# Kernel tuning notes

Measured on AMD Instinct MI355X. Metric: run time of the kernel, lower is better.

Reference implementation:

```python
import jax, jax.numpy as jnp
import numpy as np

VOCAB = 25
HIDDEN = 512
B, S = 64, 2048


def setup_inputs() -> dict:
    key = jax.random.key(0)
    ks = jax.random.split(key, 8)
    tokens = jax.random.randint(ks[0], (B, S), 0, VOCAB)
    lengths = jax.random.randint(ks[1], (B,), 1, S + 1)  # pack_padded requires length >= 1
    k = 1.0 / np.sqrt(HIDDEN)
    u = lambda kk, shp: jax.random.uniform(kk, shp, jnp.float32, -k, k)
    return {
        "tokens": tokens,
        "lengths": lengths,
        "W_ih": u(ks[2], (4 * HIDDEN, VOCAB)),   # gate order i,f,g,o (PyTorch)
        "W_hh": u(ks[3], (4 * HIDDEN, HIDDEN)),
        "b_ih": u(ks[4], (4 * HIDDEN,)),
        "b_hh": u(ks[5], (4 * HIDDEN,)),
        "fc_w": u(ks[6], (1, HIDDEN)),
        "fc_b": u(ks[7], (1,)),
    }


def _lstm_last_hidden(x, lengths, W_ih, W_hh, b_ih, b_hh):
    # x: [B,S,V] one-hot; returns h at each sequence's last valid step (packed-LSTM semantics)
    b, s, _ = x.shape
    h0 = jnp.zeros((b, HIDDEN), x.dtype)
    c0 = jnp.zeros((b, HIDDEN), x.dtype)
    # precompute input projections for all steps: [S,B,4H]
    xg = jnp.einsum('bsv,gv->sbg', x, W_ih) + b_ih + b_hh

    def step(carry, inp):
        h, c = carry
        xt, t = inp
        gates = xt + h @ W_hh.T
        i, f, g, o = jnp.split(gates, 4, axis=-1)
        i = jax.nn.sigmoid(i); f = jax.nn.sigmoid(f)
        g = jnp.tanh(g); o = jax.nn.sigmoid(o)
        c_new = f * c + i * g
        h_new = o * jnp.tanh(c_new)
        m = (t < lengths)[:, None]  # freeze state past sequence end
        return (jnp.where(m, h_new, h), jnp.where(m, c_new, c)), None

    (h, _), _ = jax.lax.scan(step, (h0, c0), (xg, jnp.arange(s)))
    return h


def reference(tokens, lengths, W_ih, W_hh, b_ih, b_hh, fc_w, fc_b):
    # sort by length descending, like the torch forward (output stays in sorted order)
    order = jnp.argsort(-lengths)
    toks = tokens[order]
    lens = lengths[order]
    x = jax.nn.one_hot(toks, VOCAB, dtype=jnp.float32)  # fused one-hot (replaces python loop)
    h = _lstm_last_hidden(x, lens, W_ih, W_hh, b_ih, b_hh)
    return h @ fc_w.T + fc_b  # [B,1]
```

## Files before the change

kernel.cpp:

```cpp
#include <hip/hip_runtime.h>


#define VOCAB 25
#define HIDDEN 512
#define BATCH 64
#define SEQ 2048
#define GB 16
#define NG 4
#define WPG 16
#define HSL 32
#define RWG 128
#define NTHREADS 256
#define HGQ (GB * HIDDEN / 2)

typedef short s16x8 __attribute__((ext_vector_type(8)));
typedef float f32x4 __attribute__((ext_vector_type(4)));

__device__ inline unsigned short f2bf(float x) {
  unsigned u = __float_as_uint(x);
  u += 0x7fffu + ((u >> 16) & 1u);
  return (unsigned short)(u >> 16);
}
__device__ inline float sigf(float x) { return 1.0f / (1.0f + __expf(-x)); }
__device__ inline float tanh_fast(float x) { return 2.0f / (1.0f + __expf(-2.0f * x)) - 1.0f; }

__global__ void prep_kernel(unsigned long long* hg, float* out) {
  const int i = blockIdx.x * blockDim.x + threadIdx.x;
  const int n = blockDim.x * gridDim.x;
  for (int k = i; k < 2 * NG * HGQ; k += n) hg[k] = 0ull;
  if (i < BATCH) out[i] = 0.f;
}

__global__ __launch_bounds__(NTHREADS, 1) void lstm_persistent(
    const int* __restrict__ tokens, const int* __restrict__ lengths,
    const float* __restrict__ W_ih, const float* __restrict__ W_hh,
    const float* __restrict__ b_ih, const float* __restrict__ b_hh,
    const float* __restrict__ fc_w, const float* __restrict__ fc_b,
    float* __restrict__ out, unsigned long long* hg) {
  const int tid = threadIdx.x;
  const int bid = blockIdx.x;
  const int x = bid & 7;
  const int g = x >> 1;
  const int w = ((bid >> 3) << 1) | (x & 1);

  __shared__ __align__(16) unsigned short hbuf[GB][HIDDEN + 8];
  __shared__ float gatesb[GB][RWG + 4];
  __shared__ float xgt[VOCAB][RWG + 4];
  __shared__ int lenAll[BATCH];
  __shared__ int order_[BATCH];
  __shared__ int gIdx[GB];
  __shared__ int gLen[GB];

  if (tid < BATCH) lenAll[tid] = lengths[tid];
  __syncthreads();
  if (tid < BATCH) {
    const int L = lenAll[tid];
    int r = 0;
    for (int j = 0; j < BATCH; ++j) {
      const int lj = lenAll[j];
      r += ((lj > L) || (lj == L && j < tid)) ? 1 : 0;
    }
    order_[r] = tid;
  }
  __syncthreads();
  if (tid < GB) {
    const int oi = order_[g * GB + tid];
    gIdx[tid] = oi;
    gLen[tid] = lenAll[oi];
  }
  for (int i = tid; i < GB * (HIDDEN + 8); i += NTHREADS)
    ((unsigned short*)hbuf)[i] = 0;
  for (int i = tid; i < VOCAB * RWG; i += NTHREADS) {
    const int v = i / RWG, rl = i % RWG;
    const int rg = (rl >> 5) * HIDDEN + w * HSL + (rl & 31);
    xgt[v][rl] = W_ih[rg * VOCAB + v] + b_ih[rg] + b_hh[rg];
  }
  __syncthreads();

  const int T = gLen[0];
  const int lane = tid & 63;
  const int wv = tid >> 6;
  const int m16 = lane & 15;
  const int quad = lane >> 4;

  s16x8 Bf[2][16];
#pragma unroll
  for (int nti = 0; nti < 2; ++nti) {
    const int nt = wv + 4 * nti;
    const int rl = nt * 16 + m16;
    const int rg = (rl >> 5) * HIDDEN + w * HSL + (rl & 31);
    const float* wr = W_hh + (size_t)rg * HIDDEN;
#pragma unroll
    for (int kt = 0; kt < 16; ++kt) {
      const float* p = wr + kt * 32 + quad * 8;
#pragma unroll
      for (int e = 0; e < 8; ++e) Bf[nti][kt][e] = (short)f2bf(p[e]);
    }
  }

  const int cb = tid >> 4;
  const int cs = tid & 15;
  const int jj0 = 2 * cs, jj1 = 2 * cs + 1;
  const int myLen = gLen[cb];
  const int* tokRow = tokens + (size_t)gIdx[cb] * SEQ;
  unsigned long long* const base0 = hg + (size_t)g * HGQ;
  unsigned long long* const base1 = hg + (size_t)(NG + g) * HGQ;

  float c0 = 0.f, c1 = 0.f, h0 = 0.f, h1 = 0.f;

  for (int t = 0; t < T; ++t) {
    const int tok = tokRow[t];

    if (t > 0) {
      const unsigned long long* src = ((t & 1) ? base1 : base0) + tid;
      unsigned long long q[16];
      for (;;) {
        bool ok = true;
#pragma unroll
        for (int r = 0; r < 16; ++r)
          q[r] = __hip_atomic_load(src + r * 256, __ATOMIC_RELAXED,
                                   __HIP_MEMORY_SCOPE_AGENT);
#pragma unroll
        for (int r = 0; r < 16; ++r) ok &= ((unsigned)(q[r] >> 32) == (unsigned)t);
        if (ok) break;
        __builtin_amdgcn_s_sleep(1);
      }
#pragma unroll
      for (int r = 0; r < 16; ++r)
        *(unsigned*)&hbuf[cb][r * 32 + jj0] = (unsigned)q[r];
    }
    __syncthreads();

    f32x4 acc0a = {0.f, 0.f, 0.f, 0.f}, acc0b = {0.f, 0.f, 0.f, 0.f};
    f32x4 acc1a = {0.f, 0.f, 0.f, 0.f}, acc1b = {0.f, 0.f, 0.f, 0.f};
#pragma unroll
    for (int kt = 0; kt < 16; kt += 2) {
      const s16x8 A0 = *(const s16x8*)&hbuf[m16][kt * 32 + quad * 8];
      const s16x8 A1 = *(const s16x8*)&hbuf[m16][(kt + 1) * 32 + quad * 8];
      acc0a = __builtin_amdgcn_mfma_f32_16x16x32_bf16(A0, Bf[0][kt], acc0a, 0, 0, 0);
      acc1a = __builtin_amdgcn_mfma_f32_16x16x32_bf16(A0, Bf[1][kt], acc1a, 0, 0, 0);
      acc0b = __builtin_amdgcn_mfma_f32_16x16x32_bf16(A1, Bf[0][kt + 1], acc0b, 0, 0, 0);
      acc1b = __builtin_amdgcn_mfma_f32_16x16x32_bf16(A1, Bf[1][kt + 1], acc1b, 0, 0, 0);
    }
    const f32x4 acc0 = acc0a + acc0b;
    const f32x4 acc1 = acc1a + acc1b;
#pragma unroll
    for (int v = 0; v < 4; ++v) {
      gatesb[quad * 4 + v][wv * 16 + m16] = acc0[v];
      gatesb[quad * 4 + v][(wv + 4) * 16 + m16] = acc1[v];
    }
    __syncthreads();

    const float pi0 = gatesb[cb][jj0] + xgt[tok][jj0];
    const float pf0 = gatesb[cb][32 + jj0] + xgt[tok][32 + jj0];
    const float pg0 = gatesb[cb][64 + jj0] + xgt[tok][64 + jj0];
    const float po0 = gatesb[cb][96 + jj0] + xgt[tok][96 + jj0];
    const float pi1 = gatesb[cb][jj1] + xgt[tok][jj1];
    const float pf1 = gatesb[cb][32 + jj1] + xgt[tok][32 + jj1];
    const float pg1 = gatesb[cb][64 + jj1] + xgt[tok][64 + jj1];
    const float po1 = gatesb[cb][96 + jj1] + xgt[tok][96 + jj1];
    if (t < myLen) {
      const float i0 = sigf(pi0), f0 = sigf(pf0), g0 = tanh_fast(pg0), o0 = sigf(po0);
      c0 = f0 * c0 + i0 * g0;
      h0 = o0 * tanh_fast(c0);
      const float i1 = sigf(pi1), f1 = sigf(pf1), g1 = tanh_fast(pg1), o1 = sigf(po1);
      c1 = f1 * c1 + i1 * g1;
      h1 = o1 * tanh_fast(c1);
    }
    if (t + 1 < T) {
      const unsigned payload = (unsigned)f2bf(h0) | ((unsigned)f2bf(h1) << 16);
      const unsigned long long qv = ((unsigned long long)(unsigned)(t + 1) << 32) | payload;
      unsigned long long* hp = (((t + 1) & 1) ? base1 : base0) + w * 256 + tid;
      __hip_atomic_store(hp, qv, __ATOMIC_RELAXED, __HIP_MEMORY_SCOPE_AGENT);
    }
  }

  float part = h0 * fc_w[w * HSL + jj0] + h1 * fc_w[w * HSL + jj1];
  part += __shfl_down(part, 8, 16);
  part += __shfl_down(part, 4, 16);
  part += __shfl_down(part, 2, 16);
  part += __shfl_down(part, 1, 16);
  if (cs == 0) {
    if (w == 0) part += fc_b[0];
    atomicAdd(&out[g * GB + cb], part);
  }
}

extern "C" void kernel_launch(void* const* d_in, const int* in_sizes, int n_in,
                              void* d_out, int out_size, void* d_ws, size_t ws_size,
                              hipStream_t stream) {
  (void)in_sizes; (void)n_in; (void)out_size; (void)ws_size;
  const int* tokens = (const int*)d_in[0];
  const int* lengths = (const int*)d_in[1];
  const float* W_ih = (const float*)d_in[2];
  const float* W_hh = (const float*)d_in[3];
  const float* b_ih = (const float*)d_in[4];
  const float* b_hh = (const float*)d_in[5];
  const float* fc_w = (const float*)d_in[6];
  const float* fc_b = (const float*)d_in[7];
  float* out = (float*)d_out;
  unsigned long long* hglob = (unsigned long long*)d_ws;

  prep_kernel<<<32, 256, 0, stream>>>(hglob, out);
  lstm_persistent<<<64, NTHREADS, 0, stream>>>(tokens, lengths, W_ih, W_hh, b_ih, b_hh,
                                               fc_w, fc_b, out, hglob);
}
```

Baseline: 5.588 ms.

## Exchange hidden state through XCD-local L2 when a group's blocks share an XCD

The launch doubles to 128 blocks and odd-indexed ones exit at once, so the 64 working blocks land on a different spread of XCDs. Each block reads its XCC id from a hardware register and publishes it, and a group whose blocks all share one XCC exchanges its per-step hidden state through a separate buffer. That buffer uses sc0 loads and stores, which stay coherent in the local L2 instead of agent-scope atomics. This aims to cut the latency of the per-timestep cross-block handoff. It adds a spin budget with fallback to the agent-scope path, duplicate stores every step, and dependence on the hardware's block-to-XCD placement.

After: 10.55 ms. 1.89x slower.

```diff
diff --git a/kernel.cpp b/kernel.cpp
--- a/kernel.cpp
+++ b/kernel.cpp
@@ -12,9 +12,12 @@
 #define RWG 128
 #define NTHREADS 256
 #define HGQ (GB * HIDDEN / 2)
+#define RC_INTS 1024
+#define L2_BUDGET 4000
 
 typedef short s16x8 __attribute__((ext_vector_type(8)));
 typedef float f32x4 __attribute__((ext_vector_type(4)));
+typedef unsigned long long ull;
 
 __device__ inline unsigned short f2bf(float x) {
   unsigned u = __float_as_uint(x);
@@ -24,10 +27,13 @@
 __device__ inline float sigf(float x) { return 1.0f / (1.0f + __expf(-x)); }
 __device__ inline float tanh_fast(float x) { return 2.0f / (1.0f + __expf(-2.0f * x)) - 1.0f; }
 
-__global__ void prep_kernel(unsigned long long* hg, float* out) {
+__global__ void prep_kernel(int* rc, ull* hgA, ull* hgL, int allow_l2, float* out) {
   const int i = blockIdx.x * blockDim.x + threadIdx.x;
   const int n = blockDim.x * gridDim.x;
-  for (int k = i; k < 2 * NG * HGQ; k += n) hg[k] = 0ull;
+  for (int k = i; k < RC_INTS; k += n) rc[k] = 0;
+  for (int k = i; k < 2 * NG * HGQ; k += n) hgA[k] = 0ull;
+  if (allow_l2)
+    for (int k = i; k < 2 * NG * HGQ; k += n) hgL[k] = 0ull;
   if (i < BATCH) out[i] = 0.f;
 }
 
@@ -36,12 +42,13 @@
     const float* __restrict__ W_ih, const float* __restrict__ W_hh,
     const float* __restrict__ b_ih, const float* __restrict__ b_hh,
     const float* __restrict__ fc_w, const float* __restrict__ fc_b,
-    float* __restrict__ out, unsigned long long* hg) {
+    float* __restrict__ out, int* rc, ull* hgA, ull* hgL, int allow_l2) {
   const int tid = threadIdx.x;
   const int bid = blockIdx.x;
   const int x = bid & 7;
+  if (x & 1) return;
   const int g = x >> 1;
-  const int w = ((bid >> 3) << 1) | (x & 1);
+  const int w = bid >> 3;
 
   __shared__ __align__(16) unsigned short hbuf[GB][HIDDEN + 8];
   __shared__ float gatesb[GB][RWG + 4];
@@ -50,6 +57,14 @@
   __shared__ int order_[BATCH];
   __shared__ int gIdx[GB];
   __shared__ int gLen[GB];
+  __shared__ int rcsh[WPG];
+
+  unsigned xcc;
+  asm volatile("s_getreg_b32 %0, hwreg(20, 0, 32)" : "=s"(xcc));
+  xcc &= 0xFu;
+  if (tid == 0)
+    __hip_atomic_store(&rc[g * WPG + w], (int)(0x100u | xcc), __ATOMIC_RELAXED,
+                       __HIP_MEMORY_SCOPE_AGENT);
 
   if (tid < BATCH) lenAll[tid] = lengths[tid];
   __syncthreads();
@@ -75,7 +90,20 @@
     const int rg = (rl >> 5) * HIDDEN + w * HSL + (rl & 31);
     xgt[v][rl] = W_ih[rg * VOCAB + v] + b_ih[rg] + b_hh[rg];
   }
+
+  if (tid < WPG) {
+    int v;
+    do {
+      v = __hip_atomic_load(&rc[g * WPG + tid], __ATOMIC_RELAXED,
+                            __HIP_MEMORY_SCOPE_AGENT);
+    } while (!(v & 0x100));
+    rcsh[tid] = v & 0xF;
+  }
   __syncthreads();
+  bool uni = true;
+#pragma unroll
+  for (int j = 0; j < WPG; ++j) uni &= (rcsh[j] == rcsh[0]);
+  const bool l2grp = uni && (allow_l2 != 0);
 
   const int T = gLen[0];
   const int lane = tid & 63;
@@ -103,27 +131,78 @@
   const int jj0 = 2 * cs, jj1 = 2 * cs + 1;
   const int myLen = gLen[cb];
   const int* tokRow = tokens + (size_t)gIdx[cb] * SEQ;
-  unsigned long long* const base0 = hg + (size_t)g * HGQ;
-  unsigned long long* const base1 = hg + (size_t)(NG + g) * HGQ;
-
+  ull* const baseA0 = hgA + (size_t)g * HGQ;
+  ull* const baseA1 = hgA + (size_t)(NG + g) * HGQ;
+  ull* const l2b0 = hgL + (size_t)g * HGQ;
+  ull* const l2b1 = hgL + (size_t)(NG + g) * HGQ;
+
+  unsigned vo[8];
+#pragma unroll
+  for (int j = 0; j < 8; ++j) vo[j] = (unsigned)(tid * 8 + j * 4096);
+  const unsigned voS = (unsigned)((w * 256 + tid) * 8);
+
+  bool l2m = l2grp;
   float c0 = 0.f, c1 = 0.f, h0 = 0.f, h1 = 0.f;
 
   for (int t = 0; t < T; ++t) {
     const int tok = tokRow[t];
 
     if (t > 0) {
-      const unsigned long long* src = ((t & 1) ? base1 : base0) + tid;
-      unsigned long long q[16];
-      for (;;) {
-        bool ok = true;
-#pragma unroll
-        for (int r = 0; r < 16; ++r)
-          q[r] = __hip_atomic_load(src + r * 256, __ATOMIC_RELAXED,
-                                   __HIP_MEMORY_SCOPE_AGENT);
-#pragma unroll
-        for (int r = 0; r < 16; ++r) ok &= ((unsigned)(q[r] >> 32) == (unsigned)t);
-        if (ok) break;
-        __builtin_amdgcn_s_sleep(1);
+      ull q[16];
+      bool got = false;
+      if (l2m) {
+        const ull* lb = (t & 1) ? l2b1 : l2b0;
+        int iters = 0;
+        for (;;) {
+          asm volatile(
+              "global_load_dwordx2 %[q0],  %[o0], %[b] sc0\n\t"
+              "global_load_dwordx2 %[q1],  %[o0], %[b] offset:2048 sc0\n\t"
+              "global_load_dwordx2 %[q2],  %[o1], %[b] sc0\n\t"
+              "global_load_dwordx2 %[q3],  %[o1], %[b] offset:2048 sc0\n\t"
+              "global_load_dwordx2 %[q4],  %[o2], %[b] sc0\n\t"
+              "global_load_dwordx2 %[q5],  %[o2], %[b] offset:2048 sc0\n\t"
+              "global_load_dwordx2 %[q6],  %[o3], %[b] sc0\n\t"
+              "global_load_dwordx2 %[q7],  %[o3], %[b] offset:2048 sc0\n\t"
+              "global_load_dwordx2 %[q8],  %[o4], %[b] sc0\n\t"
+              "global_load_dwordx2 %[q9],  %[o4], %[b] offset:2048 sc0\n\t"
+              "global_load_dwordx2 %[q10], %[o5], %[b] sc0\n\t"
+              "global_load_dwordx2 %[q11], %[o5], %[b] offset:2048 sc0\n\t"
+              "global_load_dwordx2 %[q12], %[o6], %[b] sc0\n\t"
+              "global_load_dwordx2 %[q13], %[o6], %[b] offset:2048 sc0\n\t"
+              "global_load_dwordx2 %[q14], %[o7], %[b] sc0\n\t"
+              "global_load_dwordx2 %[q15], %[o7], %[b] offset:2048 sc0\n\t"
+              "s_waitcnt vmcnt(0)"
+              : [q0] "=&v"(q[0]), [q1] "=&v"(q[1]), [q2] "=&v"(q[2]),
+                [q3] "=&v"(q[3]), [q4] "=&v"(q[4]), [q5] "=&v"(q[5]),
+                [q6] "=&v"(q[6]), [q7] "=&v"(q[7]), [q8] "=&v"(q[8]),
+                [q9] "=&v"(q[9]), [q10] "=&v"(q[10]), [q11] "=&v"(q[11]),
+                [q12] "=&v"(q[12]), [q13] "=&v"(q[13]), [q14] "=&v"(q[14]),
+                [q15] "=&v"(q[15])
+              : [o0] "v"(vo[0]), [o1] "v"(vo[1]), [o2] "v"(vo[2]),
+                [o3] "v"(vo[3]), [o4] "v"(vo[4]), [o5] "v"(vo[5]),
+                [o6] "v"(vo[6]), [o7] "v"(vo[7]), [b] "s"(lb)
+              : "memory");
+          bool ok = true;
+#pragma unroll
+          for (int r = 0; r < 16; ++r) ok &= ((unsigned)(q[r] >> 32) == (unsigned)t);
+          if (ok) { got = true; break; }
+          if (++iters > L2_BUDGET) break;
+        }
+        if (!got) l2m = false;
+      }
+      if (!got) {
+        const ull* src = ((t & 1) ? baseA1 : baseA0) + tid;
+        for (;;) {
+          bool ok = true;
+#pragma unroll
+          for (int r = 0; r < 16; ++r)
+            q[r] = __hip_atomic_load(src + r * 256, __ATOMIC_RELAXED,
+                                     __HIP_MEMORY_SCOPE_AGENT);
+#pragma unroll
+          for (int r = 0; r < 16; ++r) ok &= ((unsigned)(q[r] >> 32) == (unsigned)t);
+          if (ok) break;
+          __builtin_amdgcn_s_sleep(1);
+        }
       }
 #pragma unroll
       for (int r = 0; r < 16; ++r)
@@ -169,8 +248,13 @@
     }
     if (t + 1 < T) {
       const unsigned payload = (unsigned)f2bf(h0) | ((unsigned)f2bf(h1) << 16);
-      const unsigned long long qv = ((unsigned long long)(unsigned)(t + 1) << 32) | payload;
-      unsigned long long* hp = (((t + 1) & 1) ? base1 : base0) + w * 256 + tid;
+      const ull qv = ((ull)(unsigned)(t + 1) << 32) | payload;
+      if (l2grp) {
+        const ull* ldst = (((t + 1) & 1) ? l2b1 : l2b0);
+        asm volatile("global_store_dwordx2 %0, %1, %2 sc0"
+                     :: "v"(voS), "v"(qv), "s"(ldst) : "memory");
+      }
+      ull* hp = (((t + 1) & 1) ? baseA1 : baseA0) + w * 256 + tid;
       __hip_atomic_store(hp, qv, __ATOMIC_RELAXED, __HIP_MEMORY_SCOPE_AGENT);
     }
   }
@@ -189,7 +273,7 @@
 extern "C" void kernel_launch(void* const* d_in, const int* in_sizes, int n_in,
                               void* d_out, int out_size, void* d_ws, size_t ws_size,
                               hipStream_t stream) {
-  (void)in_sizes; (void)n_in; (void)out_size; (void)ws_size;
+  (void)in_sizes; (void)n_in; (void)out_size;
   const int* tokens = (const int*)d_in[0];
   const int* lengths = (const int*)d_in[1];
   const float* W_ih = (const float*)d_in[2];
@@ -199,9 +283,14 @@
   const float* fc_w = (const float*)d_in[6];
   const float* fc_b = (const float*)d_in[7];
   float* out = (float*)d_out;
-  unsigned long long* hglob = (unsigned long long*)d_ws;
-
-  prep_kernel<<<32, 256, 0, stream>>>(hglob, out);
-  lstm_persistent<<<64, NTHREADS, 0, stream>>>(tokens, lengths, W_ih, W_hh, b_ih, b_hh,
-                                               fc_w, fc_b, out, hglob);
-}
+
+  int* rc = (int*)d_ws;
+  ull* hgA = (ull*)((char*)d_ws + 4096);
+  ull* hgL = (ull*)((char*)d_ws + 4096 + 2 * NG * HGQ * sizeof(ull));
+  const int allow_l2 = (ws_size >= 4096 + 4ull * NG * HGQ * sizeof(ull)) ? 1 : 0;
+
+  prep_kernel<<<32, 256, 0, stream>>>(rc, hgA, hgL, allow_l2, out);
+  lstm_persistent<<<128, NTHREADS, 0, stream>>>(tokens, lengths, W_ih, W_hh, b_ih,
+                                                b_hh, fc_w, fc_b, out, rc, hgA, hgL,
+                                                allow_l2);
+}
```
